# Optimization experiments

Hardware: AMD Instinct MI355X
Metric: run time of the kernel (lower is better)

Reference implementation:

```python
import jax, jax.numpy as jnp
import numpy as np

LN_EPS = 1e-6  # flax nn.LayerNorm default


def setup_inputs() -> dict:
    key = jax.random.key(0)
    ks = jax.random.split(key, 8)
    B, N, H, D, WF = 2, 1024, 64, 32, 4
    x = jax.random.normal(ks[0], (B, N, H), jnp.float32)
    kernel_basis = jax.random.normal(ks[1], (B, N, N, D), jnp.float32)

    # chang_xavier_uniform for the kernel projection Dense (D -> H), no bias
    std = np.sqrt(2.0 / (D + H) * D).astype(np.float32)
    kernel_W = jax.random.uniform(ks[2], (D, H), jnp.float32, -std, std)
    conv_bias = jnp.zeros((H,), jnp.float32)

    ln_scale = jnp.ones((H,), jnp.float32)
    ln_bias = jnp.zeros((H,), jnp.float32)

    # flax Dense default init: lecun_normal for kernel, zeros for bias
    W1 = jax.random.normal(ks[3], (H, WF * H), jnp.float32) / np.sqrt(H).astype(np.float32)
    b1 = jnp.zeros((WF * H,), jnp.float32)
    W2 = jax.random.normal(ks[4], (WF * H, H), jnp.float32) / np.sqrt(WF * H).astype(np.float32)
    b2 = jnp.zeros((H,), jnp.float32)

    return {"x": x, "kernel_basis": kernel_basis, "kernel_W": kernel_W,
            "conv_bias": conv_bias, "ln_scale": ln_scale, "ln_bias": ln_bias,
            "W1": W1, "b1": b1, "W2": W2, "b2": b2}


def layer_norm(x, scale, bias):
    mu = jnp.mean(x, axis=-1, keepdims=True)
    var = jnp.mean(jnp.square(x - mu), axis=-1, keepdims=True)
    return (x - mu) * jax.lax.rsqrt(var + LN_EPS) * scale + bias


def reference(x, kernel_basis, kernel_W, conv_bias, ln_scale, ln_bias, W1, b1, W2, b2):
    # SepGconv: project basis (b r s d)@(d c) -> (b r s c), then contract over s
    # Fused into a single einsum so XLA can avoid materializing the full
    # (B,R,S,C) kernel if it chooses; math identical to Dense + einsum.
    a = jnp.einsum('bsc,brsd,dc->brc', x, kernel_basis, kernel_W)
    a = a + conv_bias
    # LayerNorm over channels
    a = layer_norm(a, ln_scale, ln_bias)
    # MLP with tanh-approx GELU (flax nn.gelu default)
    h = jax.nn.gelu(a @ W1 + b1, approximate=True)
    out = h @ W2 + b2
    return out
```

## Files before the change

### kernel.cpp

```cpp
#include <hip/hip_runtime.h>
#include <stdint.h>

typedef float  f32x4 __attribute__((ext_vector_type(4)));
typedef short  s16x8 __attribute__((ext_vector_type(8)));
typedef unsigned short u16;

#define KK 32768

__device__ __forceinline__ u16 f2bf_rn(float f) {
  uint32_t u = __float_as_uint(f);
  u += 0x7fffu + ((u >> 16) & 1u);
  return (u16)(u >> 16);
}
__device__ __forceinline__ float bf2f(u16 h) {
  return __uint_as_float(((uint32_t)h) << 16);
}

__device__ __forceinline__ void gload_lds16(const void* g, void* l) {
  __builtin_amdgcn_global_load_lds(
      (const __attribute__((address_space(1))) uint32_t*)g,
      (__attribute__((address_space(3))) uint32_t*)l, 16, 0, 0);
}

__global__ void build_g(const float* __restrict__ x, const float* __restrict__ W,
                        u16* __restrict__ ghi, u16* __restrict__ glo) {
  int t  = blockIdx.x * 256 + threadIdx.x;
  int k0 = (t & 4095) << 3;
  int c  = (t >> 12) & 63;
  int b  = t >> 18;
  int s  = k0 >> 5;
  int d0 = k0 & 31;
  float xv = x[(((b << 10) + s) << 6) + c];
  s16x8 vh, vl;
#pragma unroll
  for (int i = 0; i < 8; ++i) {
    float g = xv * W[((d0 + i) << 6) + c];
    u16 h = f2bf_rn(g);
    vh[i] = (short)h;
    vl[i] = (short)f2bf_rn(g - bf2f(h));
  }
  size_t off = (((size_t)((b << 6) + c)) << 15) + (size_t)k0;
  *reinterpret_cast<s16x8*>(ghi + off) = vh;
  *reinterpret_cast<s16x8*>(glo + off) = vl;
}

#define MFMA16(A_, B_, C_) __builtin_amdgcn_mfma_f32_16x16x32_bf16((A_), (B_), (C_), 0, 0, 0)

__global__ __launch_bounds__(512) void gemm_breg(
    const float* __restrict__ kb, const u16* __restrict__ ghi,
    const u16* __restrict__ glo, float* __restrict__ part) {
  __shared__ unsigned char lds[98304];

  const int tid = threadIdx.x;
  const int w   = tid >> 6;
  const int l   = tid & 63;
  const int lr  = l & 15;
  const int lk  = l >> 4;
  const int ks  = blockIdx.y;
  const int b   = blockIdx.z;
  const int rf  = w >> 2;
  const int cf  = w & 3;

  s16x8 BH[8], BL[8];
#pragma unroll
  for (int kf = 0; kf < 8; ++kf) {
    size_t off = (((size_t)((b << 6) + (cf << 4) + lr)) << 15)
               + (size_t)((ks << 8) + (kf << 5) + (lk << 3));
    BH[kf] = *reinterpret_cast<const s16x8*>(ghi + off);
    BL[kf] = *reinterpret_cast<const s16x8*>(glo + off);
  }

  const float* asrc[4];
#pragma unroll
  for (int i = 0; i < 4; ++i) {
    int row = 4 * w + i;
    int cs  = (l << 4) ^ ((row & 7) << 4);
    asrc[i] = kb + (((size_t)((b << 10) + row)) << 15)
                 + (size_t)(ks << 8) + (size_t)(cs >> 2);
  }
  const int ldst = (w << 12);

  const int r     = (rf << 4) + lr;
  const int rbase = r << 10;
  const int rswz  = (r & 7) << 4;

  float* const pbase = part + (((size_t)((b << 7) + ks)) << 16);

#define STAGE(MT_) do {                                                       \
    size_t moff_ = (size_t)(MT_) << 20;         \
    _Pragma("unroll")                                                         \
    for (int i = 0; i < 4; ++i)                                               \
      gload_lds16(asrc[i] + moff_, lds + ((MT_) % 3) * 32768 + ldst + (i << 10)); \
  } while (0)

  STAGE(0);
  STAGE(1);

  for (int mt = 0; mt < 32; ++mt) {
    if (mt == 0)       asm volatile("s_waitcnt vmcnt(4)" ::: "memory");
    else if (mt == 1)  asm volatile("s_waitcnt vmcnt(8)" ::: "memory");
    else if (mt == 31) asm volatile("s_waitcnt vmcnt(8)" ::: "memory");
    else               asm volatile("s_waitcnt vmcnt(12)" ::: "memory");
    __builtin_amdgcn_sched_barrier(0);
    __builtin_amdgcn_s_barrier();
    if (mt + 2 < 32) STAGE(mt + 2);

    const unsigned char* LA = lds + (mt % 3) * 32768;
    f32x4 acc = {0.f, 0.f, 0.f, 0.f};
#pragma unroll
    for (int kf = 0; kf < 8; ++kf) {
      int cb = (kf << 7) + (lk << 5);
      f32x4 a0 = *reinterpret_cast<const f32x4*>(LA + rbase + ( cb       ^ rswz));
      f32x4 a1 = *reinterpret_cast<const f32x4*>(LA + rbase + ((cb + 16) ^ rswz));
      s16x8 ah, al;
#pragma unroll
      for (int e = 0; e < 8; ++e) {
        float f = (e < 4) ? a0[e] : a1[e - 4];
        uint32_t u = __float_as_uint(f);
        ((short*)&ah)[e] = (short)(u16)(u >> 16);
        ((short*)&al)[e] = (short)f2bf_rn(f - __uint_as_float(u & 0xffff0000u));
      }
      acc = MFMA16(ah, BH[kf], acc);
      acc = MFMA16(al, BH[kf], acc);
      acc = MFMA16(ah, BL[kf], acc);
    }

    float* pp = pbase + (((size_t)((mt << 5) + (rf << 4) + (lk << 2))) << 6)
                      + (cf << 4) + lr;
#pragma unroll
    for (int i = 0; i < 4; ++i) pp[(size_t)i << 6] = acc[i];
  }
#undef STAGE
}

__device__ __forceinline__ float gelu_tanh(float v) {
  float u = 0.7978845608028654f * (v + 0.044715f * v * v * v);
  float e = __expf(2.0f * u);
  float th = 1.0f - 2.0f / (e + 1.0f);
  return 0.5f * v * (1.0f + th);
}

__global__ __launch_bounds__(256) void epilogue(
    const float* __restrict__ part, const float* __restrict__ conv_bias,
    const float* __restrict__ ln_scale, const float* __restrict__ ln_bias,
    const float* __restrict__ W1, const float* __restrict__ b1,
    const float* __restrict__ W2, const float* __restrict__ b2,
    float* __restrict__ out, int Sk) {
  __shared__ float red[4][64];
  __shared__ float nbuf[64];
  __shared__ float hbuf[256];

  const int tid = threadIdx.x;
  const int b = blockIdx.x >> 10;
  const int r = blockIdx.x & 1023;
  const int c = tid & 63;
  const int q = tid >> 6;

  float s = 0.0f;
  for (int ks = q; ks < Sk; ks += 4)
    s += part[(((size_t)(b * Sk + ks)) << 16) + ((size_t)r << 6) + c];
  red[q][c] = s;
  __syncthreads();

  if (q == 0) {
    float a = red[0][c] + red[1][c] + red[2][c] + red[3][c] + conv_bias[c];
    float sum = a;
#pragma unroll
    for (int off = 32; off >= 1; off >>= 1) sum += __shfl_xor(sum, off);
    float mu = sum * (1.0f / 64.0f);
    float d = a - mu;
    float ss = d * d;
#pragma unroll
    for (int off = 32; off >= 1; off >>= 1) ss += __shfl_xor(ss, off);
    float var = ss * (1.0f / 64.0f);
    nbuf[c] = d * rsqrtf(var + 1e-6f) * ln_scale[c] + ln_bias[c];
  }
  __syncthreads();

  {
    float acc = b1[tid];
#pragma unroll 8
    for (int cc = 0; cc < 64; ++cc) acc += nbuf[cc] * W1[(cc << 8) + tid];
    hbuf[tid] = gelu_tanh(acc);
  }
  __syncthreads();

  {
    float po = 0.0f;
#pragma unroll 8
    for (int jj = 0; jj < 64; ++jj) {
      int j = (q << 6) + jj;
      po += hbuf[j] * W2[(j << 6) + c];
    }
    red[q][c] = po;
  }
  __syncthreads();
  if (tid < 64) {
    float o = red[0][c] + red[1][c] + red[2][c] + red[3][c] + b2[c];
    out[(((size_t)(b << 10) + r) << 6) + c] = o;
  }
}

extern "C" void kernel_launch(void* const* d_in, const int* in_sizes, int n_in,
                              void* d_out, int out_size, void* d_ws, size_t ws_size,
                              hipStream_t stream) {
  const float* x         = (const float*)d_in[0];
  const float* kb        = (const float*)d_in[1];
  const float* kernel_W  = (const float*)d_in[2];
  const float* conv_bias = (const float*)d_in[3];
  const float* ln_scale  = (const float*)d_in[4];
  const float* ln_bias   = (const float*)d_in[5];
  const float* W1        = (const float*)d_in[6];
  const float* b1        = (const float*)d_in[7];
  const float* W2        = (const float*)d_in[8];
  const float* b2        = (const float*)d_in[9];
  float* out = (float*)d_out;

  char* wsb = (char*)d_ws;
  u16* ghi = (u16*)wsb;
  u16* glo = (u16*)(wsb + 8388608);
  float* part = (float*)(wsb + 16777216);
  const int Sk = 128;

  build_g<<<2048, 256, 0, stream>>>(x, kernel_W, ghi, glo);
  gemm_breg<<<dim3(1, Sk, 2), 512, 0, stream>>>(kb, ghi, glo, part);
  epilogue<<<dim3(2048), 256, 0, stream>>>(part, conv_bias, ln_scale, ln_bias,
                                           W1, b1, W2, b2, out, Sk);
}
```

Before: 102.2 us.

## Split GEMM rows across two workgroups with double-buffered LDS and packed bf16 conversion

Doubles the grid by splitting the 1024 output rows into two halves per workgroup, so each block runs 16 tiles instead of 32. LDS shrinks from a triple buffer to a double buffer (64KB), which could allow two workgroups per CU. A second barrier is added before prefetching into the freed buffer. The hi/lo bf16 split now uses the packed v_cvt_pk_bf16_f32 instruction, which makes the hi part round-to-nearest rather than truncated. The cost is more barrier synchronisation and a B fragment reload per workgroup.

```diff
diff --git a/kernel.cpp b/kernel.cpp
--- a/kernel.cpp
+++ b/kernel.cpp
@@ -20,6 +20,12 @@
   __builtin_amdgcn_global_load_lds(
       (const __attribute__((address_space(1))) uint32_t*)g,
       (__attribute__((address_space(3))) uint32_t*)l, 16, 0, 0);
+}
+
+__device__ __forceinline__ uint32_t cvt_pk_bf16(float lo, float hi) {
+  uint32_t r;
+  asm("v_cvt_pk_bf16_f32 %0, %1, %2" : "=v"(r) : "v"(lo), "v"(hi));
+  return r;
 }
 
 __global__ void build_g(const float* __restrict__ x, const float* __restrict__ W,
@@ -46,16 +52,17 @@
 
 #define MFMA16(A_, B_, C_) __builtin_amdgcn_mfma_f32_16x16x32_bf16((A_), (B_), (C_), 0, 0, 0)
 
-__global__ __launch_bounds__(512) void gemm_breg(
+__global__ __launch_bounds__(512) void gemm_2wg(
     const float* __restrict__ kb, const u16* __restrict__ ghi,
     const u16* __restrict__ glo, float* __restrict__ part) {
-  __shared__ unsigned char lds[98304];
+  __shared__ unsigned char lds[65536];
 
   const int tid = threadIdx.x;
   const int w   = tid >> 6;
   const int l   = tid & 63;
   const int lr  = l & 15;
   const int lk  = l >> 4;
+  const int rh  = blockIdx.x;
   const int ks  = blockIdx.y;
   const int b   = blockIdx.z;
   const int rf  = w >> 2;
@@ -73,60 +80,66 @@
   const float* asrc[4];
 #pragma unroll
   for (int i = 0; i < 4; ++i) {
-    int row = 4 * w + i;
-    int cs  = (l << 4) ^ ((row & 7) << 4);
-    asrc[i] = kb + (((size_t)((b << 10) + row)) << 15)
+    int sr = 4 * w + i;
+    int cs = (l << 4) ^ ((sr & 7) << 4);
+    asrc[i] = kb + (((size_t)((b << 10) + (rh << 9) + sr)) << 15)
                  + (size_t)(ks << 8) + (size_t)(cs >> 2);
   }
-  const int ldst = (w << 12);
 
   const int r     = (rf << 4) + lr;
   const int rbase = r << 10;
   const int rswz  = (r & 7) << 4;
-
   float* const pbase = part + (((size_t)((b << 7) + ks)) << 16);
 
-#define STAGE(MT_) do {                                                       \
-    size_t moff_ = (size_t)(MT_) << 20;         \
+#define STAGE(T_) do {                                                        \
+    size_t moff_ = (size_t)(T_) << 20;           \
     _Pragma("unroll")                                                         \
     for (int i = 0; i < 4; ++i)                                               \
-      gload_lds16(asrc[i] + moff_, lds + ((MT_) % 3) * 32768 + ldst + (i << 10)); \
+      gload_lds16(asrc[i] + moff_,                                            \
+                  lds + ((T_) & 1) * 32768 + ((4 * w + i) << 10));            \
   } while (0)
 
   STAGE(0);
   STAGE(1);
 
-  for (int mt = 0; mt < 32; ++mt) {
-    if (mt == 0)       asm volatile("s_waitcnt vmcnt(4)" ::: "memory");
-    else if (mt == 1)  asm volatile("s_waitcnt vmcnt(8)" ::: "memory");
-    else if (mt == 31) asm volatile("s_waitcnt vmcnt(8)" ::: "memory");
-    else               asm volatile("s_waitcnt vmcnt(12)" ::: "memory");
+  for (int t = 0; t < 16; ++t) {
+    if (t == 0)       asm volatile("s_waitcnt vmcnt(4)" ::: "memory");
+    else if (t == 1)  asm volatile("s_waitcnt vmcnt(8)" ::: "memory");
+    else if (t == 15) asm volatile("s_waitcnt vmcnt(8)" ::: "memory");
+    else              asm volatile("s_waitcnt vmcnt(12)" ::: "memory");
     __builtin_amdgcn_sched_barrier(0);
     __builtin_amdgcn_s_barrier();
-    if (mt + 2 < 32) STAGE(mt + 2);
-
-    const unsigned char* LA = lds + (mt % 3) * 32768;
+
+    const unsigned char* LA = lds + (t & 1) * 32768;
     f32x4 acc = {0.f, 0.f, 0.f, 0.f};
 #pragma unroll
     for (int kf = 0; kf < 8; ++kf) {
       int cb = (kf << 7) + (lk << 5);
       f32x4 a0 = *reinterpret_cast<const f32x4*>(LA + rbase + ( cb       ^ rswz));
       f32x4 a1 = *reinterpret_cast<const f32x4*>(LA + rbase + ((cb + 16) ^ rswz));
-      s16x8 ah, al;
-#pragma unroll
-      for (int e = 0; e < 8; ++e) {
-        float f = (e < 4) ? a0[e] : a1[e - 4];
-        uint32_t u = __float_as_uint(f);
-        ((short*)&ah)[e] = (short)(u16)(u >> 16);
-        ((short*)&al)[e] = (short)f2bf_rn(f - __uint_as_float(u & 0xffff0000u));
+      uint32_t hp[4], lp[4];
+#pragma unroll
+      for (int j = 0; j < 4; ++j) {
+        float f0 = (j < 2) ? a0[2 * j]     : a1[2 * j - 4];
+        float f1 = (j < 2) ? a0[2 * j + 1] : a1[2 * j - 3];
+        hp[j] = cvt_pk_bf16(f0, f1);
+        float r0 = f0 - __uint_as_float(hp[j] << 16);
+        float r1 = f1 - __uint_as_float(hp[j] & 0xffff0000u);
+        lp[j] = cvt_pk_bf16(r0, r1);
       }
+      s16x8 ah = *reinterpret_cast<s16x8*>(hp);
+      s16x8 al = *reinterpret_cast<s16x8*>(lp);
       acc = MFMA16(ah, BH[kf], acc);
       acc = MFMA16(al, BH[kf], acc);
       acc = MFMA16(ah, BL[kf], acc);
     }
-
-    float* pp = pbase + (((size_t)((mt << 5) + (rf << 4) + (lk << 2))) << 6)
-                      + (cf << 4) + lr;
+    __builtin_amdgcn_s_barrier();
+
+    if (t + 2 < 16) STAGE(t + 2);
+
+    float* pp = pbase
+              + (((size_t)((rh << 9) + (t << 5) + (rf << 4) + (lk << 2))) << 6)
+              + (cf << 4) + lr;
 #pragma unroll
     for (int i = 0; i < 4; ++i) pp[(size_t)i << 6] = acc[i];
   }
@@ -223,7 +236,7 @@
   const int Sk = 128;
 
   build_g<<<2048, 256, 0, stream>>>(x, kernel_W, ghi, glo);
-  gemm_breg<<<dim3(1, Sk, 2), 512, 0, stream>>>(kb, ghi, glo, part);
+  gemm_2wg<<<dim3(2, Sk, 2), 512, 0, stream>>>(kb, ghi, glo, part);
   epilogue<<<dim3(2048), 256, 0, stream>>>(part, conv_bias, ln_scale, ln_bias,
                                            W1, b1, W2, b2, out, Sk);
 }
```

Measured after the change: 105.2 us. 1.03x slower.
